# Performance work log

Measured on AMD Instinct MI355X. Metric: run time of the kernel, lower is better.

Reference implementation:

```python
import jax, jax.numpy as jnp
import numpy as np

EPS = 1e-6
NUM_ITERS = 8
TEMPERATURE = 1.0


def setup_inputs() -> dict:
    key = jax.random.key(0)
    k1, k2 = jax.random.split(key)
    x = jax.random.normal(k1, (4, 8192, 4096), dtype=jnp.float32)
    # nn.Linear(dim, num_experts, bias=False) weight: [num_experts, dim]
    w_gate = jax.random.normal(k2, (64, 4096), dtype=jnp.float32) * (1.0 / np.sqrt(4096))
    return {"x": x, "w_gate": w_gate}


def sinkhorn(t, num_iters=NUM_ITERS, temperature=TEMPERATURE, eps=EPS):
    # t: [b, n, e] raw gate logits (pre-log)
    t = jnp.log(jnp.clip(t, eps))  # log(clamp(t, min=eps))
    t = t / temperature
    for _ in range(num_iters):
        t = t - jax.nn.logsumexp(t, axis=-2, keepdims=True)  # normalize over tokens
        t = t - jax.nn.logsumexp(t, axis=-1, keepdims=True)  # normalize over experts
    return jnp.exp(t)


def reference(x, w_gate):
    # gate projection: [b, n, d] @ [e, d]^T -> [b, n, e]
    gates = jnp.einsum('bnd,ed->bne', x, w_gate)
    return sinkhorn(gates)
```

## Files before the change

### kernel.cpp

```cpp
#include <hip/hip_runtime.h>
#include <hip/hip_fp16.h>

#define B_ 4
#define N_ 8192
#define D_ 4096
#define E_ 64
#define M_ (B_ * N_)
#define NK 64

typedef _Float16 half8 __attribute__((ext_vector_type(8)));
typedef float f32x4 __attribute__((ext_vector_type(4)));

union H4 { _Float16 h[4]; uint2 u2; };

__global__ __launch_bounds__(256) void convert_w(const float* __restrict__ w,
                                                 _Float16* __restrict__ w16) {
  const int i = (blockIdx.x * 256 + threadIdx.x) * 4;
  const float4 v = *(const float4*)&w[i];
  H4 h;
  h.h[0] = (_Float16)v.x; h.h[1] = (_Float16)v.y;
  h.h[2] = (_Float16)v.z; h.h[3] = (_Float16)v.w;
  *(uint2*)&w16[i] = h.u2;
}

__global__ __launch_bounds__(256, 2) void gemm_log(const float* __restrict__ x,
                                                   const _Float16* __restrict__ w16,
                                                   float* __restrict__ t0,
                                                   float* __restrict__ slot0) {
  __shared__ float As[2][64 * 64];

  const int tid = threadIdx.x;
  const int lane = tid & 63;
  const int wv = tid >> 6;
  const int l15 = lane & 15;
  const int lq = lane >> 4;
  const int rowBase = blockIdx.x * 64;
  const int b = rowBase >> 13;
  const int wm = wv * 16;

  const _Float16* wB = w16 + (size_t)l15 * D_ + lq * 8;

  const int srow = wv * 4 + (lane >> 4);
#define STAGE(KC, BUF)                                                         \
  do {                                                                         \
    _Pragma("unroll")                                                          \
    for (int g = 0; g < 4; ++g) {                                              \
      const int r_ = g * 16 + srow;                                            \
      const int u_ = (lane & 15) ^ (r_ & 15);                                  \
      const float* src_ = x + (size_t)(rowBase + r_) * D_ + (KC) * 64 + u_ * 4;\
      __builtin_amdgcn_global_load_lds(                                        \
          (const __attribute__((address_space(1))) void*)src_,                 \
          (__attribute__((address_space(3))) void*)&As[BUF][(g * 16 + wv * 4) * 64], \
          16, 0, 0);                                                           \
    }                                                                          \
  } while (0)

  f32x4 acc[4] = {};

  STAGE(0, 0);
  STAGE(1, 1);

  for (int kc = 0; kc < NK; ++kc) {
    const int cur = kc & 1;
    if (kc < NK - 1) asm volatile("s_waitcnt vmcnt(4)" ::: "memory");
    else             asm volatile("s_waitcnt vmcnt(0)" ::: "memory");
    __builtin_amdgcn_s_barrier();

    half8 bfr[8];
#pragma unroll
    for (int ni = 0; ni < 4; ++ni) {
      bfr[ni * 2 + 0] = *(const half8*)(wB + (size_t)ni * 16 * D_ + kc * 64);
      bfr[ni * 2 + 1] = *(const half8*)(wB + (size_t)ni * 16 * D_ + kc * 64 + 32);
    }

    const int row = wm + l15;
    const int rm = row & 15;
#pragma unroll
    for (int ks = 0; ks < 2; ++ks) {
      const int v0 = ks * 8 + lq * 2;
      const f32x4 p0 = *(const f32x4*)&As[cur][row * 64 + ((v0 ^ rm) << 2)];
      const f32x4 p1 = *(const f32x4*)&As[cur][row * 64 + (((v0 + 1) ^ rm) << 2)];
      half8 af;
      af[0] = (_Float16)p0[0]; af[1] = (_Float16)p0[1];
      af[2] = (_Float16)p0[2]; af[3] = (_Float16)p0[3];
      af[4] = (_Float16)p1[0]; af[5] = (_Float16)p1[1];
      af[6] = (_Float16)p1[2]; af[7] = (_Float16)p1[3];
#pragma unroll
      for (int ni = 0; ni < 4; ++ni)
        acc[ni] = __builtin_amdgcn_mfma_f32_16x16x32_f16(af, bfr[ni * 2 + ks], acc[ni], 0, 0, 0);
    }

    asm volatile("s_waitcnt lgkmcnt(0)" ::: "memory");
    __builtin_amdgcn_s_barrier();

    if (kc + 2 < NK) STAGE(kc + 2, cur);
  }
#undef STAGE

#pragma unroll
  for (int ni = 0; ni < 4; ++ni) {
    float lsum = 0.f;
#pragma unroll
    for (int r = 0; r < 4; ++r) {
      const float v = fmaxf(acc[ni][r], 1e-6f);
      const int grow = rowBase + wm + lq * 4 + r;
      const int gcol = ni * 16 + l15;
      t0[(size_t)grow * E_ + gcol] = __logf(v);
      lsum += v;
    }
    float v = lsum;
    v += __shfl_xor(v, 16);
    v += __shfl_xor(v, 32);
    if (lq == 0) atomicAdd(&slot0[b * E_ + ni * 16 + l15], v);
  }
}

__global__ __launch_bounds__(256) void sinkhorn_iter(const float* __restrict__ t0,
                                                     float* __restrict__ slots,
                                                     float* __restrict__ out,
                                                     int it, int last) {
  const int tid = threadIdx.x;
  const int lane = tid & 63;
  const int wv = tid >> 6;
  const int b = blockIdx.x >> 8;
  const int chunk = blockIdx.x & 255;

  float C = __logf(slots[b * E_ + lane]);
  for (int j = 1; j < it; ++j) C += __logf(slots[j * (B_ * E_) + b * E_ + lane]);

  float colacc = 0.f;
  const int nbase = chunk * 32 + wv * 8;
#pragma unroll
  for (int i = 0; i < 8; ++i) {
    const int n = nbase + i;
    const float v = t0[((size_t)b * N_ + n) * E_ + lane];
    const float p = __expf(v - C);
    float s = p;
    s += __shfl_xor(s, 1);  s += __shfl_xor(s, 2);  s += __shfl_xor(s, 4);
    s += __shfl_xor(s, 8);  s += __shfl_xor(s, 16); s += __shfl_xor(s, 32);
    const float q = p / s;
    if (last) out[((size_t)b * N_ + n) * E_ + lane] = q;
    else      colacc += q;
  }
  if (!last) {
    __shared__ float wsum[4][64];
    wsum[wv][lane] = colacc;
    __syncthreads();
    if (tid < 64) {
      const float tot = wsum[0][tid] + wsum[1][tid] + wsum[2][tid] + wsum[3][tid];
      atomicAdd(&slots[it * (B_ * E_) + b * E_ + tid], tot);
    }
  }
}

extern "C" void kernel_launch(void* const* d_in, const int* in_sizes, int n_in,
                              void* d_out, int out_size, void* d_ws, size_t ws_size,
                              hipStream_t stream) {
  (void)in_sizes; (void)n_in; (void)out_size; (void)ws_size;
  const float* x = (const float*)d_in[0];
  const float* w = (const float*)d_in[1];
  float* out = (float*)d_out;
  float* slots = (float*)d_ws;
  _Float16* w16 = (_Float16*)((char*)d_ws + 8192);

  hipMemsetAsync(slots, 0, 8 * B_ * E_ * sizeof(float), stream);
  convert_w<<<(E_ * D_) / 1024, 256, 0, stream>>>(w, w16);
  gemm_log<<<M_ / 64, 256, 0, stream>>>(x, w16, out, slots);
  for (int it = 1; it <= 8; ++it)
    sinkhorn_iter<<<B_ * 256, 256, 0, stream>>>(out, slots, out, it, it == 8 ? 1 : 0);
}
```

Measured before the change: 264.0 us.

## Stage x through registers as fp16 in LDS with 512-thread 2x4 wave tiling

Replaces direct global-to-LDS fp32 staging with register-prefetched loads that convert x to fp16 before writing to LDS. This halves LDS footprint and read traffic. The block grows to 512 threads with waves split over both M and N, so each wave loads fewer weight fragments. Column sums are now reduced in shared memory before one atomic per expert instead of four. In exchange it uses a single-stage register prefetch rather than the two-buffer async pipeline, so load latency may be exposed.

```diff
diff --git a/kernel.cpp b/kernel.cpp
--- a/kernel.cpp
+++ b/kernel.cpp
@@ -23,95 +23,100 @@
   *(uint2*)&w16[i] = h.u2;
 }
 
-__global__ __launch_bounds__(256, 2) void gemm_log(const float* __restrict__ x,
+__global__ __launch_bounds__(512, 4) void gemm_log(const float* __restrict__ x,
                                                    const _Float16* __restrict__ w16,
                                                    float* __restrict__ t0,
                                                    float* __restrict__ slot0) {
-  __shared__ float As[2][64 * 64];
+  __shared__ _Float16 As[2][64 * 64];
+  __shared__ float wsum[8][32];
 
   const int tid = threadIdx.x;
   const int lane = tid & 63;
   const int wv = tid >> 6;
+  const int wm = (wv >> 1) * 16;
+  const int wn = (wv & 1) * 32;
   const int l15 = lane & 15;
   const int lq = lane >> 4;
   const int rowBase = blockIdx.x * 64;
   const int b = rowBase >> 13;
-  const int wm = wv * 16;
 
-  const _Float16* wB = w16 + (size_t)l15 * D_ + lq * 8;
+  const int sr = tid >> 3;
+  const int su = tid & 7;
+  const float* xs = x + (size_t)(rowBase + sr) * D_ + su * 8;
+  const int sdst = sr * 64 + ((su ^ (sr & 7)) << 3);
 
-  const int srow = wv * 4 + (lane >> 4);
-#define STAGE(KC, BUF)                                                         \
-  do {                                                                         \
-    _Pragma("unroll")                                                          \
-    for (int g = 0; g < 4; ++g) {                                              \
-      const int r_ = g * 16 + srow;                                            \
-      const int u_ = (lane & 15) ^ (r_ & 15);                                  \
-      const float* src_ = x + (size_t)(rowBase + r_) * D_ + (KC) * 64 + u_ * 4;\
-      __builtin_amdgcn_global_load_lds(                                        \
-          (const __attribute__((address_space(1))) void*)src_,                 \
-          (__attribute__((address_space(3))) void*)&As[BUF][(g * 16 + wv * 4) * 64], \
-          16, 0, 0);                                                           \
-    }                                                                          \
-  } while (0)
+  const int arow = wm + l15;
+  const int aoff0 = arow * 64 + (((0 * 4 + lq) ^ (arow & 7)) << 3);
+  const int aoff1 = arow * 64 + (((1 * 4 + lq) ^ (arow & 7)) << 3);
 
-  f32x4 acc[4] = {};
+  const _Float16* wB0 = w16 + (size_t)(wn + l15) * D_ + lq * 8;
+  const _Float16* wB1 = w16 + (size_t)(wn + 16 + l15) * D_ + lq * 8;
 
-  STAGE(0, 0);
-  STAGE(1, 1);
+  f32x4 acc0 = {}, acc1 = {};
+  float4 xa, xb;
+  half8 b00, b01, b10, b11;
+
+  xa = *(const float4*)(xs);
+  xb = *(const float4*)(xs + 4);
 
   for (int kc = 0; kc < NK; ++kc) {
     const int cur = kc & 1;
-    if (kc < NK - 1) asm volatile("s_waitcnt vmcnt(4)" ::: "memory");
-    else             asm volatile("s_waitcnt vmcnt(0)" ::: "memory");
-    __builtin_amdgcn_s_barrier();
+    const int ko = kc * 64;
 
-    half8 bfr[8];
-#pragma unroll
-    for (int ni = 0; ni < 4; ++ni) {
-      bfr[ni * 2 + 0] = *(const half8*)(wB + (size_t)ni * 16 * D_ + kc * 64);
-      bfr[ni * 2 + 1] = *(const half8*)(wB + (size_t)ni * 16 * D_ + kc * 64 + 32);
-    }
+    b00 = *(const half8*)(wB0 + ko);
+    b01 = *(const half8*)(wB0 + ko + 32);
+    b10 = *(const half8*)(wB1 + ko);
+    b11 = *(const half8*)(wB1 + ko + 32);
 
-    const int row = wm + l15;
-    const int rm = row & 15;
-#pragma unroll
-    for (int ks = 0; ks < 2; ++ks) {
-      const int v0 = ks * 8 + lq * 2;
-      const f32x4 p0 = *(const f32x4*)&As[cur][row * 64 + ((v0 ^ rm) << 2)];
-      const f32x4 p1 = *(const f32x4*)&As[cur][row * 64 + (((v0 + 1) ^ rm) << 2)];
-      half8 af;
-      af[0] = (_Float16)p0[0]; af[1] = (_Float16)p0[1];
-      af[2] = (_Float16)p0[2]; af[3] = (_Float16)p0[3];
-      af[4] = (_Float16)p1[0]; af[5] = (_Float16)p1[1];
-      af[6] = (_Float16)p1[2]; af[7] = (_Float16)p1[3];
-#pragma unroll
-      for (int ni = 0; ni < 4; ++ni)
-        acc[ni] = __builtin_amdgcn_mfma_f32_16x16x32_f16(af, bfr[ni * 2 + ks], acc[ni], 0, 0, 0);
+    half8 hx;
+    hx[0] = (_Float16)xa.x; hx[1] = (_Float16)xa.y;
+    hx[2] = (_Float16)xa.z; hx[3] = (_Float16)xa.w;
+    hx[4] = (_Float16)xb.x; hx[5] = (_Float16)xb.y;
+    hx[6] = (_Float16)xb.z; hx[7] = (_Float16)xb.w;
+    *(half8*)&As[cur][sdst] = hx;
+
+    if (kc + 1 < NK) {
+      xa = *(const float4*)(xs + ko + 64);
+      xb = *(const float4*)(xs + ko + 68);
     }
 
     asm volatile("s_waitcnt lgkmcnt(0)" ::: "memory");
     __builtin_amdgcn_s_barrier();
 
-    if (kc + 2 < NK) STAGE(kc + 2, cur);
+    half8 a0 = *(const half8*)&As[cur][aoff0];
+    half8 a1 = *(const half8*)&As[cur][aoff1];
+    acc0 = __builtin_amdgcn_mfma_f32_16x16x32_f16(a0, b00, acc0, 0, 0, 0);
+    acc0 = __builtin_amdgcn_mfma_f32_16x16x32_f16(a1, b01, acc0, 0, 0, 0);
+    acc1 = __builtin_amdgcn_mfma_f32_16x16x32_f16(a0, b10, acc1, 0, 0, 0);
+    acc1 = __builtin_amdgcn_mfma_f32_16x16x32_f16(a1, b11, acc1, 0, 0, 0);
   }
-#undef STAGE
 
+  float ls0 = 0.f, ls1 = 0.f;
 #pragma unroll
-  for (int ni = 0; ni < 4; ++ni) {
-    float lsum = 0.f;
-#pragma unroll
-    for (int r = 0; r < 4; ++r) {
-      const float v = fmaxf(acc[ni][r], 1e-6f);
-      const int grow = rowBase + wm + lq * 4 + r;
-      const int gcol = ni * 16 + l15;
-      t0[(size_t)grow * E_ + gcol] = __logf(v);
-      lsum += v;
-    }
-    float v = lsum;
-    v += __shfl_xor(v, 16);
-    v += __shfl_xor(v, 32);
-    if (lq == 0) atomicAdd(&slot0[b * E_ + ni * 16 + l15], v);
+  for (int r = 0; r < 4; ++r) {
+    const float v0 = fmaxf(acc0[r], 1e-6f);
+    const float v1 = fmaxf(acc1[r], 1e-6f);
+    const int grow = rowBase + wm + lq * 4 + r;
+    t0[(size_t)grow * E_ + wn + l15] = __logf(v0);
+    t0[(size_t)grow * E_ + wn + 16 + l15] = __logf(v1);
+    ls0 += v0; ls1 += v1;
+  }
+  {
+    float vv = ls0;
+    vv += __shfl_xor(vv, 16); vv += __shfl_xor(vv, 32);
+    if (lq == 0) wsum[wv][l15] = vv;
+    vv = ls1;
+    vv += __shfl_xor(vv, 16); vv += __shfl_xor(vv, 32);
+    if (lq == 0) wsum[wv][16 + l15] = vv;
+  }
+  __syncthreads();
+  if (tid < 64) {
+    const int e = tid;
+    const int half = e >> 5;
+    const int idx = e & 31;
+    const float tot = wsum[0 * 2 + half][idx] + wsum[1 * 2 + half][idx] +
+                      wsum[2 * 2 + half][idx] + wsum[3 * 2 + half][idx];
+    atomicAdd(&slot0[b * E_ + e], tot);
   }
 }
 
@@ -165,7 +170,7 @@
 
   hipMemsetAsync(slots, 0, 8 * B_ * E_ * sizeof(float), stream);
   convert_w<<<(E_ * D_) / 1024, 256, 0, stream>>>(w, w16);
-  gemm_log<<<M_ / 64, 256, 0, stream>>>(x, w16, out, slots);
+  gemm_log<<<M_ / 64, 512, 0, stream>>>(x, w16, out, slots);
   for (int it = 1; it <= 8; ++it)
     sinkhorn_iter<<<B_ * 256, 256, 0, stream>>>(out, slots, out, it, it == 8 ? 1 : 0);
 }
```

Result: faster. 253.6 us (-3.9%).
